# Kernel tuning notes

Hardware: AMD Instinct MI355X
Metric: run time of the kernel (lower is better)

The kernel has to match this reference:

```python
import jax, jax.numpy as jnp
import numpy as np

N, E, C, L = 50000, 625000, 128, 4
H = 2 * C  # hidden size of per-layer ObjectModel
FRAC_SCALE = 1.0 / 16.0   # fractional_bitwidth = 4
Q_MAX = 8.0               # int_bitwidth = 4 -> signed fixed point range [-8, 8 - 1/16]


def fq(x):
    """Fixed-point fake-quantize (4 int bits, 4 frac bits, signed)."""
    return jnp.clip(jnp.round(x / FRAC_SCALE) * FRAC_SCALE, -Q_MAX, Q_MAX - FRAC_SCALE)


def qlin(h, W, b):
    # QuantLinear: input/weight/bias/output all quantized
    return fq(fq(h) @ fq(W) + fq(b))


def qbn(h, w, b):
    # BatchNorm1dToQuantScaleBias in inference: per-channel scale + bias
    return fq(fq(h) * fq(w) + fq(b))


def setup_inputs() -> dict:
    key = jax.random.key(0)
    ks = jax.random.split(key, 24)
    d = {}
    d["x"] = jax.random.normal(ks[0], (N, 3), dtype=jnp.float32)
    d["edge_attr"] = jax.random.normal(ks[1], (E, 4), dtype=jnp.float32)
    d["edge_index"] = jax.random.randint(ks[2], (2, E), 0, N, dtype=jnp.int64)
    # encoders
    d["node_W"] = jax.random.normal(ks[3], (3, C), dtype=jnp.float32) * 0.4
    d["node_b"] = jax.random.normal(ks[4], (C,), dtype=jnp.float32) * 0.2
    d["edge_W"] = jax.random.normal(ks[5], (4, C), dtype=jnp.float32) * 0.4
    d["edge_b"] = jax.random.normal(ks[6], (C,), dtype=jnp.float32) * 0.2
    d["node_bn_w"] = 1.0 + 0.1 * jax.random.normal(ks[7], (C,), dtype=jnp.float32)
    d["node_bn_b"] = 0.1 * jax.random.normal(ks[8], (C,), dtype=jnp.float32)
    d["edge_bn_w"] = 1.0 + 0.1 * jax.random.normal(ks[9], (C,), dtype=jnp.float32)
    d["edge_bn_b"] = 0.1 * jax.random.normal(ks[10], (C,), dtype=jnp.float32)
    # per-layer ObjectModel params (stacked over L)
    d["W1"] = jax.random.normal(ks[11], (L, C, H), dtype=jnp.float32) * (0.5 / np.sqrt(C))
    d["b1"] = jax.random.normal(ks[12], (L, H), dtype=jnp.float32) * 0.1
    d["bn_w"] = 1.0 + 0.1 * jax.random.normal(ks[13], (L, H), dtype=jnp.float32)
    d["bn_b"] = 0.1 * jax.random.normal(ks[14], (L, H), dtype=jnp.float32)
    d["W2"] = jax.random.normal(ks[15], (L, H, C), dtype=jnp.float32) * (0.5 / np.sqrt(H))
    d["b2"] = jax.random.normal(ks[16], (L, C), dtype=jnp.float32) * 0.1
    d["fc_W"] = jax.random.normal(ks[17], (C, 1), dtype=jnp.float32) * (0.5 / np.sqrt(C))
    d["fc_b"] = jax.random.normal(ks[18], (1,), dtype=jnp.float32) * 0.1
    return d


def reference(x, edge_attr, edge_index, node_W, node_b, edge_W, edge_b,
              node_bn_w, node_bn_b, edge_bn_w, edge_bn_b,
              W1, b1, bn_w, bn_b, W2, b2, fc_W, fc_b):
    src = edge_index[0]  # x_j (source) under flow='source_to_target'
    tgt = edge_index[1]  # aggregation target i

    h = fq(qlin(x, node_W, node_b))            # node encoder [N, C]
    e = fq(qlin(edge_attr, edge_W, edge_b))    # edge encoder [E, C]
    h = qbn(h, node_bn_w, node_bn_b)
    e = qbn(e, edge_bn_w, edge_bn_b)

    for l in range(L):
        # message: quant(x_j) + quant(edge_attr), QuantReLU
        msg = fq(jax.nn.relu(fq(h[src]) + fq(e)))          # [E, C]
        agg = jax.ops.segment_sum(msg, tgt, num_segments=N)  # scatter-sum [N, C]
        u = fq(agg)
        # ObjectModel: QuantLinear -> ScaleBias BN -> QuantReLU -> QuantLinear, then QuantIdentity
        z = qlin(u, W1[l], b1[l])
        z = qbn(z, bn_w[l], bn_b[l])
        z = fq(jax.nn.relu(z))
        z = fq(qlin(z, W2[l], b2[l]))
        h = h + z                                           # residual

    pooled = jnp.mean(h, axis=0, keepdims=True)  # global_mean_pool, batch=None -> [1, C]
    out = qlin(fq(pooled), fc_W, fc_b)           # [1, 1]
    out = fq(jax.nn.sigmoid(fq(out)))            # QuantSigmoid
    return out.reshape(-1)                       # [1]
```

## Files before the change

### kernel.cpp

```cpp
#include <hip/hip_runtime.h>
#include <stdint.h>

#define NN 50000
#define EE 625000
#define EPAD (EE + 16)
#define CC 128
#define HH 256
#define LL 4
#define NPAD 50048
#define NBLK (NPAD/64)
#define R2 32

typedef __attribute__((ext_vector_type(4))) int   i32x4;

__device__ __forceinline__ float qbf(float x){
  return fminf(127.f, fmaxf(-128.f, rintf(x*16.f)));
}
__device__ __forceinline__ float rq16(float t){
  return fminf(127.f, fmaxf(-128.f, rintf(t*0.0625f)));
}

__global__ void k_qbig(const float* __restrict__ W1, const float* __restrict__ W2,
                       signed char* __restrict__ w1q8, signed char* __restrict__ w2q8){
  int i = blockIdx.x*256 + threadIdx.x;
  if (i >= LL*CC*HH) return;
  {
    float v = qbf(W1[i]);
    int l = i / (CC*HH); int r = i - l*CC*HH; int c = r / HH; int hh = r - c*HH;
    w1q8[((size_t)l*HH + hh)*CC + c] = (signed char)v;
  }
  {
    float v = qbf(W2[i]);
    int l = i / (HH*CC); int r = i - l*HH*CC; int hh = r / CC; int c = r - hh*CC;
    w2q8[((size_t)l*CC + c)*HH + hh] = (signed char)v;
  }
}

struct QS { const float* s; float* d; int n; float m; };
struct QSArgs { QS q[14]; };

__global__ void k_qsmall(QSArgs a){
  for (int r=0;r<14;++r){
    QS qs = a.q[r];
    for (int i = blockIdx.x*blockDim.x + threadIdx.x; i < qs.n; i += gridDim.x*blockDim.x)
      qs.d[i] = qs.m * qbf(qs.s[i]);
  }
}

__global__ void k_epack(const float* __restrict__ ewf, const float* __restrict__ eb16,
                        const float* __restrict__ ebnw, const float* __restrict__ ebnb16,
                        float4* __restrict__ epA, float4* __restrict__ epB){
  int c = threadIdx.x;
  epA[c] = make_float4(ewf[c], ewf[CC+c], ewf[2*CC+c], ewf[3*CC+c]);
  epB[c] = make_float4(eb16[c], ebnw[c], ebnb16[c], 0.f);
}

__global__ __launch_bounds__(256) void k_node_enc(
    const float* __restrict__ x, const float* __restrict__ nW,
    const float* __restrict__ nb16, const float* __restrict__ bnw,
    const float* __restrict__ bnb16, short* __restrict__ h0,
    signed char* __restrict__ hq8){
  int idx = blockIdx.x*256 + threadIdx.x;
  int n = idx >> 7, c = idx & 127;
  float x0 = qbf(x[n*3]), x1 = qbf(x[n*3+1]), x2 = qbf(x[n*3+2]);
  float S = x0*nW[c] + x1*nW[CC+c] + x2*nW[2*CC+c];
  float v1 = rq16(S + nb16[c]);
  float v2 = rq16(v1*bnw[c] + bnb16[c]);
  h0[idx] = (short)v2;
  hq8[idx] = (signed char)v2;
}

__global__ void k_deg(const int* __restrict__ ei, int* __restrict__ deg){
  int e = blockIdx.x*256 + threadIdx.x;
  if (e < EE) atomicAdd(&deg[ei[EE + e]], 1);
}

__global__ __launch_bounds__(256) void k_scanA(const int* __restrict__ deg,
                                               int* __restrict__ offI,
                                               int* __restrict__ btot){
  __shared__ int sh[256];
  int t = threadIdx.x;
  int base = blockIdx.x*1024 + t*4;
  int v[4]; int s = 0;
  #pragma unroll
  for (int i=0;i<4;++i){ v[i] = (base+i < NN) ? deg[base+i] : 0; s += v[i]; }
  sh[t] = s; __syncthreads();
  for (int off=1; off<256; off<<=1){
    int xv = (t>=off) ? sh[t-off] : 0;
    __syncthreads();
    sh[t] += xv;
    __syncthreads();
  }
  int run = (t>0) ? sh[t-1] : 0;
  #pragma unroll
  for (int i=0;i<4;++i){ run += v[i]; if (base+i < NN) offI[base+i] = run; }
  if (t==255) btot[blockIdx.x] = sh[255];
}

__global__ void k_scanB(const int* __restrict__ btot, int* __restrict__ boff, int nblk){
  if (threadIdx.x==0 && blockIdx.x==0){
    int run = 0;
    for (int b=0;b<nblk;++b){ int v = btot[b]; boff[b] = run; run += v; }
  }
}

__global__ void k_scanC(const int* __restrict__ boff, const int* __restrict__ deg,
                        int* __restrict__ offI, int* __restrict__ cursor){
  int i = blockIdx.x*256 + threadIdx.x;
  if (i < NN){
    int v = offI[i] + boff[i>>10];
    offI[i] = v;
    cursor[i] = v - deg[i];
  }
}

__global__ __launch_bounds__(256) void k_fill(
    const int* __restrict__ ei, const float* __restrict__ ea,
    const float4* __restrict__ epA, const float4* __restrict__ epB,
    int* __restrict__ cursor, int* __restrict__ srcoff,
    signed char* __restrict__ eq){
  int e = blockIdx.x*256 + threadIdx.x;
  if (e >= EE) return;
  int tgt = ei[EE + e];
  int p = atomicAdd(&cursor[tgt], 1);
  srcoff[p] = ei[e] * CC;
  float4 v = ((const float4*)ea)[e];
  float qx = qbf(v.x), qy = qbf(v.y), qz = qbf(v.z), qw = qbf(v.w);
  signed char* row = eq + ((size_t)p << 7);
  #pragma unroll
  for (int c16 = 0; c16 < 8; ++c16){
    int out[4];
    #pragma unroll
    for (int c4 = 0; c4 < 4; ++c4){
      uint packed = 0;
      #pragma unroll
      for (int jj = 0; jj < 4; ++jj){
        int c = c16*16 + c4*4 + jj;
        float4 A = epA[c]; float4 B = epB[c];
        float S  = qx*A.x + qy*A.y + qz*A.z + qw*A.w;
        float v1 = rq16(S + B.x);
        float ec = rq16(v1*B.y + B.z);
        packed |= ((uint)((int)ec & 0xff)) << (8*jj);
      }
      out[c4] = (int)packed;
    }
    *(int4*)(row + c16*16) = make_int4(out[0], out[1], out[2], out[3]);
  }
}

__global__ __launch_bounds__(256) void k_msg(
    const int* __restrict__ offI, const int* __restrict__ deg_,
    const int* __restrict__ srcoff, const signed char* __restrict__ eq,
    const signed char* __restrict__ hq8, signed char* __restrict__ uq){
  int n = blockIdx.x*4 + (threadIdx.x >> 6);
  int lane = threadIdx.x & 63;
  int c0 = lane*2;
  int end = offI[n];
  int start = end - deg_[n];
  int acc0 = 0, acc1 = 0;
  for (int base = start; base < end; base += 16){
    int rem = end - base;
    int so = srcoff[base + min(lane, rem-1)];
    ushort hv[16], ev[16];
    #pragma unroll
    for (int j=0;j<16;++j){
      int soj = __builtin_amdgcn_readlane(so, j);
      hv[j] = *(const ushort*)(hq8 + soj + c0);
      ev[j] = *(const ushort*)(eq + (((size_t)(base+j)) << 7) + c0);
    }
    #pragma unroll
    for (int j=0;j<16;++j){
      if (j < rem){
        int h0 = ((int)hv[j] << 24) >> 24;
        int h1 = ((int)(short)hv[j]) >> 8;
        int e0 = ((int)ev[j] << 24) >> 24;
        int e1 = ((int)(short)ev[j]) >> 8;
        acc0 += min(max(h0 + e0, 0), 127);
        acc1 += min(max(h1 + e1, 0), 127);
      }
    }
  }
  int ua = min(acc0, 127), ub = min(acc1, 127);
  *(ushort*)(uq + (size_t)n*CC + c0) = (ushort)((ua & 0xff) | ((ub & 0xff) << 8));
}

__global__ __launch_bounds__(256, 3) void k_om(
    int l, const signed char* __restrict__ uq,
    const signed char* __restrict__ w1q8, const float* __restrict__ b1q16,
    const float* __restrict__ bnwf, const float* __restrict__ bnb16,
    const signed char* __restrict__ w2q8, const float* __restrict__ b2q16,
    const short* __restrict__ h_in, short* __restrict__ h_out,
    signed char* __restrict__ hq8, int* __restrict__ partial){
  __shared__ signed char uL[64][144];
  __shared__ signed char zL[64][272];
  int t = threadIdx.x;
  int nb = blockIdx.x * 64;
  {
    const i32x4* src = (const i32x4*)(uq + (size_t)nb*CC + t*32);
    int flat = t*32; int r = flat >> 7, c = flat & 127;
    *(i32x4*)&uL[r][c]      = src[0];
    *(i32x4*)&uL[r][c + 16] = src[1];
  }
  int lane = t & 63, wv = t >> 6;
  int lr = lane & 15, lk = lane >> 4;
  const signed char* W1p = w1q8 + (size_t)l*HH*CC;
  i32x4 w1f[2][4];
  #pragma unroll
  for (int ks=0; ks<2; ++ks)
    #pragma unroll
    for (int ci=0; ci<4; ++ci)
      w1f[ks][ci] = *(const i32x4*)(W1p + (size_t)(wv*64 + ci*16 + lr)*CC + ks*64 + lk*16);
  __syncthreads();

  i32x4 acc[4][4];
  #pragma unroll
  for (int mi=0;mi<4;++mi)
    #pragma unroll
    for (int ci=0;ci<4;++ci) acc[mi][ci] = (i32x4){0,0,0,0};
  #pragma unroll
  for (int ks=0; ks<2; ++ks){
    i32x4 av[4];
    #pragma unroll
    for (int mi=0;mi<4;++mi) av[mi] = *(const i32x4*)&uL[mi*16+lr][ks*64 + lk*16];
    #pragma unroll
    for (int mi=0;mi<4;++mi)
      #pragma unroll
      for (int ci=0;ci<4;++ci)
        acc[mi][ci] = __builtin_amdgcn_mfma_i32_16x16x64_i8(av[mi], w1f[ks][ci], acc[mi][ci], 0,0,0);
  }
  #pragma unroll
  for (int ci=0;ci<4;++ci){
    int hcol = wv*64 + ci*16 + lr;
    float b1 = b1q16[l*HH + hcol];
    float bw = bnwf[l*HH + hcol];
    float bb = bnb16[l*HH + hcol];
    #pragma unroll
    for (int mi=0;mi<4;++mi){
      #pragma unroll
      for (int r=0;r<4;++r){
        float v1 = rq16((float)acc[mi][ci][r] + b1);
        float v2 = fmaxf(rq16(v1*bw + bb), 0.f);
        zL[mi*16 + lk*4 + r][hcol] = (signed char)v2;
      }
    }
  }
  const signed char* W2p = w2q8 + (size_t)l*CC*HH;
  i32x4 w2f[4][2];
  #pragma unroll
  for (int ks=0; ks<4; ++ks)
    #pragma unroll
    for (int ci=0; ci<2; ++ci)
      w2f[ks][ci] = *(const i32x4*)(W2p + (size_t)(wv*32 + ci*16 + lr)*HH + ks*64 + lk*16);
  __syncthreads();

  i32x4 a2[4][2];
  #pragma unroll
  for (int mi=0;mi<4;++mi){ a2[mi][0] = (i32x4){0,0,0,0}; a2[mi][1] = (i32x4){0,0,0,0}; }
  #pragma unroll
  for (int ks=0; ks<4; ++ks){
    i32x4 av[4];
    #pragma unroll
    for (int mi=0;mi<4;++mi) av[mi] = *(const i32x4*)&zL[mi*16+lr][ks*64 + lk*16];
    #pragma unroll
    for (int mi=0;mi<4;++mi)
      #pragma unroll
      for (int ci=0;ci<2;++ci)
        a2[mi][ci] = __builtin_amdgcn_mfma_i32_16x16x64_i8(av[mi], w2f[ks][ci], a2[mi][ci], 0,0,0);
  }
  int psum[2] = {0, 0};
  #pragma unroll
  for (int ci=0;ci<2;++ci){
    int ccol = wv*32 + ci*16 + lr;
    float b2 = b2q16[l*CC + ccol];
    #pragma unroll
    for (int mi=0;mi<4;++mi){
      #pragma unroll
      for (int r=0;r<4;++r){
        int node = nb + mi*16 + lk*4 + r;
        float v = rq16((float)a2[mi][ci][r] + b2);
        int hn = (int)h_in[(size_t)node*CC + ccol] + (int)v;
        if (node < NN){
          h_out[(size_t)node*CC + ccol] = (short)hn;
          hq8[(size_t)node*CC + ccol] = (signed char)min(max(hn, -128), 127);
          psum[ci] += hn;
        }
      }
    }
  }
  if (partial){
    #pragma unroll
    for (int ci=0;ci<2;++ci){
      int s = psum[ci];
      s += __shfl_xor(s, 16);
      s += __shfl_xor(s, 32);
      if (lk == 0)
        partial[blockIdx.x*CC + wv*32 + ci*16 + lr] = s;
    }
  }
}

__global__ __launch_bounds__(256) void k_red(
    const int* __restrict__ partial, int* __restrict__ partial2){
  int t = threadIdx.x;
  int c = t & 127;
  int sub = blockIdx.x*2 + (t >> 7);
  int s = 0;
  for (int b = sub; b < NBLK; b += R2) s += partial[b*CC + c];
  partial2[sub*CC + c] = s;
}

__global__ __launch_bounds__(256) void k_final(
    const int* __restrict__ partial2, const float* __restrict__ fcwf,
    const float* __restrict__ fcb16, float* __restrict__ out){
  __shared__ int ired[128];
  __shared__ float red[128];
  int t = threadIdx.x;
  int c = t & 127, half = t >> 7;
  int s = 0;
  #pragma unroll
  for (int b = half; b < R2; b += 2) s += partial2[b*CC + c];
  if (half) ired[c] = s;
  __syncthreads();
  if (!half){
    int sc = s + ired[c];
    double m = (double)sc / (double)NN;
    float pq = fminf(127.f, fmaxf(-128.f, (float)rint(m)));
    red[c] = pq * fcwf[c];
  }
  __syncthreads();
  for (int o=64;o>0;o>>=1){ if (t<o) red[t] += red[t+o]; __syncthreads(); }
  if (t==0){
    float v = rq16(red[0] + fcb16[0]);
    float o1 = v * 0.0625f;
    float sg = 1.f/(1.f + expf(-o1));
    float oq = fminf(127.f, fmaxf(-128.f, rintf(sg*16.f)));
    out[0] = oq * 0.0625f;
  }
}

extern "C" void kernel_launch(void* const* d_in, const int* in_sizes, int n_in,
                              void* d_out, int out_size, void* d_ws, size_t ws_size,
                              hipStream_t stream){
  (void)in_sizes; (void)n_in; (void)out_size; (void)ws_size;
  const float* x   = (const float*)d_in[0];
  const float* ea  = (const float*)d_in[1];
  const int*   ei  = (const int*)d_in[2];
  const float* W1  = (const float*)d_in[11];
  const float* W2  = (const float*)d_in[15];

  char* w = (char*)d_ws;
  auto alloc = [&](size_t bytes)->char*{
    char* p = w; w += (bytes + 255) & ~(size_t)255; return p;
  };
  short* h0        = (short*)alloc((size_t)NPAD*CC*2);
  short* h1        = (short*)alloc((size_t)NPAD*CC*2);
  signed char* hq8 = (signed char*)alloc((size_t)NPAD*CC);
  signed char* uq  = (signed char*)alloc((size_t)NPAD*CC);
  int* srcoff      = (int*)alloc((size_t)EPAD*4);
  int* deg         = (int*)alloc(NN*4);
  int* offI        = (int*)alloc(NN*4);
  int* cursor      = (int*)alloc(NN*4);
  int* btot        = (int*)alloc(64*4);
  int* boff        = (int*)alloc(64*4);
  int* partial     = (int*)alloc((size_t)NBLK*CC*4);
  int* partial2    = (int*)alloc((size_t)R2*CC*4);
  signed char* w1q8= (signed char*)alloc((size_t)LL*CC*HH);
  signed char* w2q8= (signed char*)alloc((size_t)LL*CC*HH);
  float* nodeWf    = (float*)alloc(3*CC*4);
  float* nb16f     = (float*)alloc(CC*4);
  float* nbnwf     = (float*)alloc(CC*4);
  float* nbnb16f   = (float*)alloc(CC*4);
  float* ewf       = (float*)alloc(4*CC*4);
  float* eb16f     = (float*)alloc(CC*4);
  float* ebnwf     = (float*)alloc(CC*4);
  float* ebnb16f   = (float*)alloc(CC*4);
  float* b1q16f    = (float*)alloc(LL*HH*4);
  float* bnwf      = (float*)alloc(LL*HH*4);
  float* bnb16f    = (float*)alloc(LL*HH*4);
  float* b2q16f    = (float*)alloc(LL*CC*4);
  float* fcwf      = (float*)alloc(CC*4);
  float* fcb16f    = (float*)alloc(256);
  float4* epA      = (float4*)alloc(CC*16);
  float4* epB      = (float4*)alloc(CC*16);
  signed char* eq  = (signed char*)alloc((size_t)EPAD*CC);

  hipMemsetAsync(deg, 0, NN*4, stream);

  k_qbig<<<(LL*CC*HH + 255)/256, 256, 0, stream>>>(W1, W2, w1q8, w2q8);

  QSArgs qa;
  auto setq = [&](int r, int idx, float* d, int n, float m){
    qa.q[r].s = (const float*)d_in[idx]; qa.q[r].d = d; qa.q[r].n = n; qa.q[r].m = m;
  };
  setq(0, 3,  nodeWf,  3*CC, 1.f);
  setq(1, 4,  nb16f,   CC,   16.f);
  setq(2, 5,  ewf,     4*CC, 1.f);
  setq(3, 6,  eb16f,   CC,   16.f);
  setq(4, 7,  nbnwf,   CC,   1.f);
  setq(5, 8,  nbnb16f, CC,   16.f);
  setq(6, 9,  ebnwf,   CC,   1.f);
  setq(7, 10, ebnb16f, CC,   16.f);
  setq(8, 12, b1q16f,  LL*HH, 16.f);
  setq(9, 13, bnwf,    LL*HH, 1.f);
  setq(10,14, bnb16f,  LL*HH, 16.f);
  setq(11,16, b2q16f,  LL*CC, 16.f);
  setq(12,17, fcwf,    CC,   1.f);
  setq(13,18, fcb16f,  1,    16.f);
  k_qsmall<<<4, 256, 0, stream>>>(qa);
  k_epack<<<1, 128, 0, stream>>>(ewf, eb16f, ebnwf, ebnb16f, epA, epB);

  k_node_enc<<<(NN*CC)/256, 256, 0, stream>>>(x, nodeWf, nb16f, nbnwf, nbnb16f, h0, hq8);
  k_deg<<<(EE+255)/256, 256, 0, stream>>>(ei, deg);
  int nblk = (NN + 1023)/1024;
  k_scanA<<<nblk, 256, 0, stream>>>(deg, offI, btot);
  k_scanB<<<1, 64, 0, stream>>>(btot, boff, nblk);
  k_scanC<<<(NN+255)/256, 256, 0, stream>>>(boff, deg, offI, cursor);
  k_fill<<<(EE+255)/256, 256, 0, stream>>>(ei, ea, epA, epB, cursor, srcoff, eq);

  for (int l=0;l<LL;++l){
    const short* hi = (l & 1) ? h1 : h0;
    short* ho       = (l & 1) ? h0 : h1;
    k_msg<<<NN/4, 256, 0, stream>>>(offI, deg, srcoff, eq, hq8, uq);
    k_om<<<NBLK, 256, 0, stream>>>(l, uq, w1q8, b1q16f, bnwf, bnb16f,
                                   w2q8, b2q16f, hi, ho, hq8,
                                   (l == LL-1) ? partial : nullptr);
  }
  k_red<<<R2/2, 256, 0, stream>>>(partial, partial2);
  k_final<<<1, 256, 0, stream>>>(partial2, fcwf, fcb16f, (float*)d_out);
}
```

Measured before the change: 360.8 us.

## Split edge encoding from CSR fill and index edge features by original id

The CSR fill kernel previously wrote each encoded 128-byte edge row at its sorted position, so every scattered thread wrote a full row. Now the fill writes only an (src offset, edge offset) pair per slot. A separate coalesced grid-stride kernel encodes edge features in original edge order, with each group of 32 threads covering one row. In exchange, the message kernel must gather edge rows through the indirection in all four layers instead of reading them sequentially, which costs locality and an extra readlane per edge.

```diff
diff --git a/kernel.cpp b/kernel.cpp
--- a/kernel.cpp
+++ b/kernel.cpp
@@ -114,43 +114,44 @@
   }
 }
 
-__global__ __launch_bounds__(256) void k_fill(
-    const int* __restrict__ ei, const float* __restrict__ ea,
+__global__ void k_fill(const int* __restrict__ ei, int* __restrict__ cursor,
+                       int2* __restrict__ adj){
+  int e = blockIdx.x*256 + threadIdx.x;
+  if (e < EE){
+    int tgt = ei[EE + e];
+    int p = atomicAdd(&cursor[tgt], 1);
+    adj[p] = make_int2(ei[e] * CC, e * CC);
+  }
+}
+
+__global__ __launch_bounds__(256) void k_eenc(
+    const float* __restrict__ ea,
     const float4* __restrict__ epA, const float4* __restrict__ epB,
-    int* __restrict__ cursor, int* __restrict__ srcoff,
     signed char* __restrict__ eq){
-  int e = blockIdx.x*256 + threadIdx.x;
-  if (e >= EE) return;
-  int tgt = ei[EE + e];
-  int p = atomicAdd(&cursor[tgt], 1);
-  srcoff[p] = ei[e] * CC;
-  float4 v = ((const float4*)ea)[e];
-  float qx = qbf(v.x), qy = qbf(v.y), qz = qbf(v.z), qw = qbf(v.w);
-  signed char* row = eq + ((size_t)p << 7);
-  #pragma unroll
-  for (int c16 = 0; c16 < 8; ++c16){
-    int out[4];
-    #pragma unroll
-    for (int c4 = 0; c4 < 4; ++c4){
-      uint packed = 0;
-      #pragma unroll
-      for (int jj = 0; jj < 4; ++jj){
-        int c = c16*16 + c4*4 + jj;
-        float4 A = epA[c]; float4 B = epB[c];
-        float S  = qx*A.x + qy*A.y + qz*A.z + qw*A.w;
-        float v1 = rq16(S + B.x);
-        float ec = rq16(v1*B.y + B.z);
-        packed |= ((uint)((int)ec & 0xff)) << (8*jj);
-      }
-      out[c4] = (int)packed;
-    }
-    *(int4*)(row + c16*16) = make_int4(out[0], out[1], out[2], out[3]);
+  int t = blockIdx.x*256 + threadIdx.x;
+  int c0 = (t & 31) * 4;
+  float4 A[4], B[4];
+  #pragma unroll
+  for (int j=0;j<4;++j){ A[j] = epA[c0+j]; B[j] = epB[c0+j]; }
+  int stride = (gridDim.x*256) >> 5;
+  for (int p = t >> 5; p < EE; p += stride){
+    float4 v = ((const float4*)ea)[p];
+    float qx = qbf(v.x), qy = qbf(v.y), qz = qbf(v.z), qw = qbf(v.w);
+    uint packed = 0;
+    #pragma unroll
+    for (int j=0;j<4;++j){
+      float S  = qx*A[j].x + qy*A[j].y + qz*A[j].z + qw*A[j].w;
+      float v1 = rq16(S + B[j].x);
+      float ec = rq16(v1*B[j].y + B[j].z);
+      packed |= ((uint)((int)ec & 0xff)) << (8*j);
+    }
+    *(uint*)(eq + ((size_t)p << 7) + c0) = packed;
   }
 }
 
 __global__ __launch_bounds__(256) void k_msg(
     const int* __restrict__ offI, const int* __restrict__ deg_,
-    const int* __restrict__ srcoff, const signed char* __restrict__ eq,
+    const int2* __restrict__ adj, const signed char* __restrict__ eq,
     const signed char* __restrict__ hq8, signed char* __restrict__ uq){
   int n = blockIdx.x*4 + (threadIdx.x >> 6);
   int lane = threadIdx.x & 63;
@@ -160,13 +161,14 @@
   int acc0 = 0, acc1 = 0;
   for (int base = start; base < end; base += 16){
     int rem = end - base;
-    int so = srcoff[base + min(lane, rem-1)];
+    int2 a = adj[base + min(lane, rem-1)];
     ushort hv[16], ev[16];
     #pragma unroll
     for (int j=0;j<16;++j){
-      int soj = __builtin_amdgcn_readlane(so, j);
+      int soj = __builtin_amdgcn_readlane(a.x, j);
+      int eoj = __builtin_amdgcn_readlane(a.y, j);
       hv[j] = *(const ushort*)(hq8 + soj + c0);
-      ev[j] = *(const ushort*)(eq + (((size_t)(base+j)) << 7) + c0);
+      ev[j] = *(const ushort*)(eq + eoj + c0);
     }
     #pragma unroll
     for (int j=0;j<16;++j){
@@ -356,7 +358,7 @@
   short* h1        = (short*)alloc((size_t)NPAD*CC*2);
   signed char* hq8 = (signed char*)alloc((size_t)NPAD*CC);
   signed char* uq  = (signed char*)alloc((size_t)NPAD*CC);
-  int* srcoff      = (int*)alloc((size_t)EPAD*4);
+  int2* adj        = (int2*)alloc((size_t)EPAD*8);
   int* deg         = (int*)alloc(NN*4);
   int* offI        = (int*)alloc(NN*4);
   int* cursor      = (int*)alloc(NN*4);
@@ -415,12 +417,13 @@
   k_scanA<<<nblk, 256, 0, stream>>>(deg, offI, btot);
   k_scanB<<<1, 64, 0, stream>>>(btot, boff, nblk);
   k_scanC<<<(NN+255)/256, 256, 0, stream>>>(boff, deg, offI, cursor);
-  k_fill<<<(EE+255)/256, 256, 0, stream>>>(ei, ea, epA, epB, cursor, srcoff, eq);
+  k_fill<<<(EE+255)/256, 256, 0, stream>>>(ei, cursor, adj);
+  k_eenc<<<2048, 256, 0, stream>>>(ea, epA, epB, eq);
 
   for (int l=0;l<LL;++l){
     const short* hi = (l & 1) ? h1 : h0;
     short* ho       = (l & 1) ? h0 : h1;
-    k_msg<<<NN/4, 256, 0, stream>>>(offI, deg, srcoff, eq, hq8, uq);
+    k_msg<<<NN/4, 256, 0, stream>>>(offI, deg, adj, eq, hq8, uq);
     k_om<<<NBLK, 256, 0, stream>>>(l, uq, w1q8, b1q16f, bnwf, bnb16f,
                                    w2q8, b2q16f, hi, ho, hq8,
                                    (l == LL-1) ? partial : nullptr);
```

After: 389.1 us. 1.08x slower.
